# Kernel tuning notes

Hardware: AMD Instinct MI355X
Metric: run time of the kernel (lower is better)

The kernel has to match this reference:

```python
import jax, jax.numpy as jnp
import numpy as np

HEADS = 8
DIM_HEAD = 32
GSS = 3
SCALE = DIM_HEAD ** -0.5
LN_EPS = 1e-5


def setup_inputs() -> dict:
    key = jax.random.key(0)
    ks = jax.random.split(key, 5)
    B, C, H, W = 16, 256, 96, 96
    inner = HEADS * DIM_HEAD  # 256
    return {
        "x": jax.random.normal(ks[0], (B, C, H, W), jnp.float32),
        "w_qkv": jax.random.normal(ks[1], (inner * 3, C), jnp.float32) * 0.02,
        "group_tokens": jax.random.normal(ks[2], (C,), jnp.float32),
        "ln_gamma": jnp.ones((DIM_HEAD,), jnp.float32),
        "ln_beta": jnp.zeros((DIM_HEAD,), jnp.float32),
        "w_qk": jax.random.normal(ks[3], (inner * 2, inner), jnp.float32) * 0.02,
        "b_qk": jnp.zeros((inner * 2,), jnp.float32),
        "w_out": jax.random.normal(ks[4], (C, inner), jnp.float32) * 0.02,
        "b_out": jnp.zeros((C,), jnp.float32),
    }


def reference(x, w_qkv, group_tokens, ln_gamma, ln_beta, w_qk, b_qk, w_out, b_out):
    B, C, H, W = x.shape
    g, h, d = GSS, HEADS, DIM_HEAD
    X, Y = H // g, W // g
    n_groups = X * Y
    bg = B * n_groups
    win = g * g  # 9 tokens per spatial window

    # 'b c (h g1) (w g2) -> (b h w) c (g1 g2)'
    xg = x.reshape(B, C, X, g, Y, g).transpose(0, 2, 4, 1, 3, 5).reshape(bg, C, win)
    # prepend learned group token
    tok = jnp.broadcast_to(group_tokens[None, :, None], (bg, C, 1))
    xg = jnp.concatenate([tok, xg], axis=-1)

    # 1x1 conv QKV projection
    qkv = jnp.einsum('oc,bcn->bon', w_qkv, xg)
    q, k, v = jnp.split(qkv, 3, axis=1)

    def to_heads(t):  # 'b (h d) n -> b h n d'
        return t.reshape(bg, h, d, win + 1).transpose(0, 1, 3, 2)
    q, k, v = map(to_heads, (q, k, v))

    dots = jnp.einsum('bhid,bhjd->bhij', q * SCALE, k)
    attn = jax.nn.softmax(dots, axis=-1)
    out = jnp.einsum('bhij,bhjd->bhid', attn, v)

    gt = out[:, :, 0]    # [bg, h, d] group tokens
    gf = out[:, :, 1:]

    # '(b x y) h d -> b h (x y) d'
    gt = gt.reshape(B, n_groups, h, d).transpose(0, 2, 1, 3)
    # '(b x y) h n d -> b h (x y) n d'
    gf = gf.reshape(B, n_groups, h, win, d).transpose(0, 2, 1, 3, 4)

    # group_tokens_to_qk: LayerNorm(d) -> GELU -> 1x1 conv on (h d) channels
    mu = gt.mean(axis=-1, keepdims=True)
    var = gt.var(axis=-1, keepdims=True)
    gtn = (gt - mu) * jax.lax.rsqrt(var + LN_EPS) * ln_gamma + ln_beta
    gtn = jax.nn.gelu(gtn, approximate=False)
    # 'b h n c -> b (h c) n'
    t = gtn.transpose(0, 1, 3, 2).reshape(B, h * d, n_groups)
    qk = jnp.einsum('oc,bcn->bon', w_qk, t) + b_qk[None, :, None]
    # 'b (h c) n -> b h n c'
    qk = qk.reshape(B, h, 2 * d, n_groups).transpose(0, 1, 3, 2)
    w_q, w_k = jnp.split(qk, 2, axis=-1)

    # stage-2 hierarchical attention over group tokens
    w_dots = jnp.einsum('bhid,bhjd->bhij', w_q * SCALE, w_k)
    w_attn = jax.nn.softmax(w_dots, axis=-1)
    agg = jnp.einsum('bhij,bhjwd->bhiwd', w_attn, gf)

    # 'b h (x y) (g1 g2) d -> b (h d) (x g1) (y g2)'
    fmap = agg.reshape(B, h, X, Y, g, g, d).transpose(0, 1, 6, 2, 4, 3, 5)
    fmap = fmap.reshape(B, h * d, H, W)

    return jnp.einsum('oc,bchw->bohw', w_out, fmap) + b_out[None, :, None, None]
```

## Files before the change

### kernel.cpp

```cpp
#include <hip/hip_runtime.h>
#include <cmath>

namespace {
constexpr int kNH = 8;
constexpr int kNG = 1024;
constexpr float kScale = 0.17677669529663687f;
}

typedef short  bf16x8 __attribute__((ext_vector_type(8)));
typedef short  bf16x4 __attribute__((ext_vector_type(4)));
typedef float  f32x4  __attribute__((ext_vector_type(4)));

__device__ __forceinline__ unsigned short f2b(float f) {
  unsigned int u = __builtin_bit_cast(unsigned int, f);
  u += 0x7fffu + ((u >> 16) & 1u);
  return (unsigned short)(u >> 16);
}
__device__ __forceinline__ float b2f(unsigned short h) {
  unsigned int u = ((unsigned int)h) << 16;
  return __builtin_bit_cast(float, u);
}
__device__ __forceinline__ int swc(int row, int col) {
  return col ^ (((row >> 3) & 3) << 3);
}

__global__ void __launch_bounds__(256) k_wcvt(const float* __restrict__ w_qkv,
                                              const float* __restrict__ w_out,
                                              unsigned short* __restrict__ wb,
                                              unsigned short* __restrict__ w_hi,
                                              unsigned short* __restrict__ w_lo) {
  int i = blockIdx.x * 256 + threadIdx.x;
  if (i < 196608) {
    wb[i] = f2b(w_qkv[i]);
  } else {
    int k = i - 196608;
    float v = w_out[k];
    unsigned short h = f2b(v);
    w_hi[k] = h;
    w_lo[k] = f2b(v - b2f(h));
  }
}

__global__ void __launch_bounds__(256) k_tok(const float* __restrict__ w_qkv,
                                             const float* __restrict__ gtok,
                                             unsigned short* __restrict__ tok_b) {
  int o = blockIdx.x * 256 + threadIdx.x;
  if (o < 768) {
    float s = 0.f;
    for (int c = 0; c < 256; ++c) s += w_qkv[o * 256 + c] * gtok[c];
    tok_b[o] = f2b(s);
  }
}

__global__ void __launch_bounds__(256, 2)
k_xt(const float* __restrict__ x, unsigned short* __restrict__ xt, int b0) {
  __shared__ short Lt[64][72];
  const int tid = threadIdx.x;
  const int bid = blockIdx.x;
  const int bb = bid / 576;
  const int r2 = bid - bb * 576;
  const int ct = r2 / 144;
  const int ptile = r2 - ct * 144;
  const int c0 = ct * 64, p0 = ptile * 64;
  const float* xb = x + ((size_t)((b0 + bb) * 256 + c0)) * 9216 + p0;
#pragma unroll
  for (int i = 0; i < 16; ++i) {
    int idx = i * 256 + tid;
    int c = idx >> 6, p = idx & 63;
    Lt[c][p] = (short)f2b(xb[(size_t)c * 9216 + p]);
  }
  __syncthreads();
  unsigned short* xto = xt + ((size_t)bb * 9216 + p0) * 256 + c0;
#pragma unroll
  for (int i = 0; i < 2; ++i) {
    int t = i * 256 + tid;
    int p = t & 63, oc = t >> 6;
    bf16x8 v8;
#pragma unroll
    for (int e = 0; e < 8; ++e) v8[e] = Lt[oc * 8 + e][p];
    *(bf16x8*)&xto[(size_t)p * 256 + oc * 8] = v8;
  }
}

__global__ void __launch_bounds__(256, 4)
k_qkv(const unsigned short* __restrict__ w_bf, const unsigned short* __restrict__ xt,
      unsigned short* __restrict__ qkv) {
  const int tid = threadIdx.x;
  const int N = gridDim.x;
  const int lg = (blockIdx.x & 7) * (N >> 3) + (blockIdx.x >> 3);
  const int pt = lg / 6;
  const int ot = lg - pt * 6;
  const int o0 = ot * 128;
  const int wv = tid >> 6, lane = tid & 63, ln = lane & 15, qq = lane >> 4;
  const int ow = (wv >> 1) * 64, pw = (wv & 1) * 64;
  const size_t prow = (size_t)pt * 128 + pw;
  const unsigned short* xbase = xt + (prow + ln) * 256;
  const unsigned short* wbase = w_bf + (size_t)(o0 + ow + ln) * 256;

  f32x4 acc[4][4];
#pragma unroll
  for (int mf = 0; mf < 4; ++mf)
#pragma unroll
    for (int nf = 0; nf < 4; ++nf) acc[mf][nf] = {0.f, 0.f, 0.f, 0.f};

  for (int ks = 0; ks < 8; ++ks) {
    const int co = ks * 32 + qq * 8;
    bf16x8 bfr[4], afr[4];
#pragma unroll
    for (int nf = 0; nf < 4; ++nf) bfr[nf] = *(const bf16x8*)&xbase[(size_t)nf * 4096 + co];
#pragma unroll
    for (int mf = 0; mf < 4; ++mf) afr[mf] = *(const bf16x8*)&wbase[(size_t)mf * 4096 + co];
#pragma unroll
    for (int mf = 0; mf < 4; ++mf)
#pragma unroll
      for (int nf = 0; nf < 4; ++nf)
        acc[mf][nf] = __builtin_amdgcn_mfma_f32_16x16x32_bf16(afr[mf], bfr[nf], acc[mf][nf], 0, 0, 0);
  }
#pragma unroll
  for (int mf = 0; mf < 4; ++mf)
#pragma unroll
    for (int nf = 0; nf < 4; ++nf) {
      bf16x4 sv;
#pragma unroll
      for (int r = 0; r < 4; ++r) sv[r] = (short)f2b(acc[mf][nf][r]);
      *(bf16x4*)&qkv[(prow + nf * 16 + ln) * 768 + o0 + ow + mf * 16 + qq * 4] = sv;
    }
}

__global__ void __launch_bounds__(256, 3)
k_attn(const unsigned short* __restrict__ qkv, const unsigned short* __restrict__ tok_b,
       const float* __restrict__ ln_g, const float* __restrict__ ln_b,
       unsigned short* __restrict__ t_b, unsigned short* __restrict__ gf_t, int b0) {
  __shared__ __align__(16) short smem[23040];
  short* vt = smem;
  short* pl = smem + 20480;

  const int tid = threadIdx.x;
  const int N = gridDim.x;
  const int lg = (blockIdx.x & 7) * (N >> 3) + (blockIdx.x >> 3);
  const int bb = lg >> 9;
  const int b  = b0 + bb;
  const int n0 = (lg & 511) * 2;
  const int wv = tid >> 6, lane = tid & 63, ln = lane & 15, qq = lane >> 4;
  const int grp = wv >> 1;
  const int n = n0 + grp;
  const size_t brow = (size_t)bb * 9216;

  {
    bf16x8 z8 = {0, 0, 0, 0, 0, 0, 0, 0};
    for (int i = 0; i < 12; ++i) {
      int off = (i * 256 + tid) * 8;
      if (off < 23040) *(bf16x8*)&smem[off] = z8;
    }
  }
  __syncthreads();

  for (int it = 0; it < 9; ++it) {
    int t = it * 256 + tid;
    if (t < 2304) {
      int win = t >= 1152 ? 1 : 0;
      int rem = t - win * 1152;
      int pix = rem >> 7, dp = rem & 127, d = dp * 2;
      int nn = n0 + win;
      int gx = nn >> 5, gy = nn & 31;
      int gi = (pix * 11) >> 5, gj = pix - 3 * gi;
      int p = (gx * 3 + gi) * 96 + gy * 3 + gj;
      unsigned int u = *(const unsigned int*)&qkv[(brow + p) * 768 + 512 + d];
      int col = pix + 1;
      int r0 = (win << 8) + d;
      vt[r0 * 40 + swc(r0, col)] = (short)(u & 0xffffu);
      vt[(r0 + 1) * 40 + swc(r0 + 1, col)] = (short)(u >> 16);
    }
  }
#pragma unroll
  for (int i = 0; i < 2; ++i) {
    int t = i * 256 + tid;
    vt[t * 40 + swc(t, 0)] = (short)tok_b[512 + (t & 255)];
  }
  __syncthreads();

  const unsigned short* rowq;
  {
    bool isPix = (ln >= 1 && ln <= 9);
    int pix = ln - 1;
    int gi = isPix ? ((pix * 11) >> 5) : 0;
    int gj = isPix ? (pix - 3 * gi) : 0;
    int gx = n >> 5, gy = n & 31;
    int p = (gx * 3 + gi) * 96 + gy * 3 + gj;
    rowq = isPix ? qkv + (brow + p) * 768 + qq * 8 : tok_b + qq * 8;
  }

  f32x4 z = {0.f, 0.f, 0.f, 0.f};
  for (int tt = 0; tt < 4; ++tt) {
    int hh = (wv & 1) * 4 + tt;
    bf16x8 aq = *(const bf16x8*)&rowq[hh * 32];
    bf16x8 bk = *(const bf16x8*)&rowq[256 + hh * 32];
    f32x4 s = __builtin_amdgcn_mfma_f32_16x16x32_bf16(aq, bk, z, 0, 0, 0);

    float pr[4], sm[4];
#pragma unroll
    for (int r = 0; r < 4; ++r) {
      float sv = s[r] * kScale;
      if (ln >= 10) sv = -1e30f;
      float mx = sv;
#pragma unroll
      for (int d = 1; d < 16; d <<= 1) mx = fmaxf(mx, __shfl_xor(mx, d));
      pr[r] = __expf(sv - mx);
      float t2 = pr[r];
#pragma unroll
      for (int d = 1; d < 16; d <<= 1) t2 += __shfl_xor(t2, d);
      sm[r] = t2;
    }
#pragma unroll
    for (int r = 0; r < 4; ++r)
      pl[wv * 640 + (qq * 4 + r) * 40 + ln] = (short)f2b(pr[r]);

    bf16x8 ap = *(const bf16x8*)&pl[wv * 640 + ln * 40 + qq * 8];
    int rv0 = (grp << 8) + hh * 32 + ln;
    int rv1 = rv0 + 16;
    bf16x8 v0 = *(const bf16x8*)&vt[rv0 * 40 + swc(rv0, qq * 8)];
    bf16x8 v1 = *(const bf16x8*)&vt[rv1 * 40 + swc(rv1, qq * 8)];
    f32x4 o0 = __builtin_amdgcn_mfma_f32_16x16x32_bf16(ap, v0, z, 0, 0, 0);
    f32x4 o1 = __builtin_amdgcn_mfma_f32_16x16x32_bf16(ap, v1, z, 0, 0, 0);

    if (qq == 0) {
      float inv0 = 1.f / sm[0];
      float va = o0[0] * inv0, vb = o1[0] * inv0;
      float ssum = va + vb;
#pragma unroll
      for (int d = 1; d < 16; d <<= 1) ssum += __shfl_xor(ssum, d);
      float mu = ssum * (1.f / 32.f);
      float dva = va - mu, dvb = vb - mu;
      float vsum = dva * dva + dvb * dvb;
#pragma unroll
      for (int d = 1; d < 16; d <<= 1) vsum += __shfl_xor(vsum, d);
      float ri = rsqrtf(vsum * (1.f / 32.f) + 1e-5f);
      float g0 = dva * ri * ln_g[ln] + ln_b[ln];
      float g1 = dvb * ri * ln_g[16 + ln] + ln_b[16 + ln];
      float e0 = 0.5f * g0 * (1.f + erff(g0 * 0.70710678118654752f));
      float e1 = 0.5f * g1 * (1.f + erff(g1 * 0.70710678118654752f));
      size_t tb = ((size_t)(b * 1024 + n)) * 256 + hh * 32 + ln;
      t_b[tb] = f2b(e0);
      t_b[tb + 16] = f2b(e1);
    }
#pragma unroll
    for (int r = 0; r < 4; ++r) {
      int i = qq * 4 + r;
      if (i >= 1 && i <= 9) {
        float inv = 1.f / sm[r];
        size_t base = ((size_t)((b * 8 + hh) * 288) + (i - 1) * 32 + ln) * 1024 + n;
        gf_t[base] = f2b(o0[r] * inv);
        gf_t[base + 16 * 1024] = f2b(o1[r] * inv);
      }
    }
  }
}

__global__ void __launch_bounds__(256, 2)
k_qk(const unsigned short* __restrict__ t_b, const float* __restrict__ w_qk,
     const float* __restrict__ b_qk, unsigned short* __restrict__ wq_b,
     unsigned short* __restrict__ wk_b) {
  __shared__ float t_l[128][33];
  __shared__ float w_l[64][33];
  int tid = threadIdx.x;
  int bid = blockIdx.x;
  int b = bid >> 6;
  int h = (bid >> 3) & 7;
  int nt = bid & 7;
  int n_base = nt * 128;
  int te = tid & 15, tn = tid >> 4;
  float accq[4][8] = {};
  for (int c0 = 0; c0 < 256; c0 += 32) {
    for (int i = 0; i < 16; ++i) {
      int nl = i * 8 + (tid >> 5);
      t_l[nl][tid & 31] = b2f(t_b[((size_t)(b * kNG) + n_base + nl) * 256 + c0 + (tid & 31)]);
    }
    for (int i = 0; i < 8; ++i) {
      int e = i * 8 + (tid >> 5);
      w_l[e][tid & 31] = w_qk[(size_t)(h * 64 + e) * 256 + c0 + (tid & 31)];
    }
    __syncthreads();
    for (int cc = 0; cc < 32; ++cc) {
      float wvv[4], tvv[8];
#pragma unroll
      for (int i = 0; i < 4; ++i) wvv[i] = w_l[te + 16 * i][cc];
#pragma unroll
      for (int j = 0; j < 8; ++j) tvv[j] = t_l[tn + 16 * j][cc];
#pragma unroll
      for (int i = 0; i < 4; ++i)
#pragma unroll
        for (int j = 0; j < 8; ++j) accq[i][j] += wvv[i] * tvv[j];
    }
    __syncthreads();
  }
#pragma unroll
  for (int i = 0; i < 4; ++i) {
    int e = te + 16 * i;
    float bias = b_qk[h * 64 + e];
#pragma unroll
    for (int j = 0; j < 8; ++j) {
      int n = n_base + tn + 16 * j;
      float v = accq[i][j] + bias;
      size_t idx = (((size_t)b * kNH + h) * kNG + n) * 32;
      if (e < 32) wq_b[idx + e] = f2b(v * kScale);
      else        wk_b[idx + (e - 32)] = f2b(v);
    }
  }
}

__global__ void __launch_bounds__(256, 3)
k_flash(const unsigned short* __restrict__ wq_b, const unsigned short* __restrict__ wk_b,
        const unsigned short* __restrict__ gf_t, unsigned short* __restrict__ agg_b) {
  __shared__ __align__(16) short vt[12800];
  __shared__ __align__(16) short pl[2560];
  __shared__ float al_l[64];
  __shared__ float lrow_l[64];

  const int tid = threadIdx.x;
  const int bid0 = blockIdx.x;
  const int xcd = bid0 & 7;
  const int s   = bid0 >> 3;
  const int bh  = xcd + 8 * (s >> 4);
  const int qt  = s & 15;
  const int wv = tid >> 6;
  const int lane = tid & 63;
  const int ln = lane & 15;
  const int qq = lane >> 4;
  const int d0 = wv * 80;

  bf16x8 aq = *(const bf16x8*)&wq_b[(size_t)(bh * 1024 + qt * 64 + wv * 16 + ln) * 32 + qq * 8];

  f32x4 accv[4][5];
  float mrow[4], lrow[4];
#pragma unroll
  for (int mf = 0; mf < 4; ++mf)
#pragma unroll
    for (int nf = 0; nf < 5; ++nf) accv[mf][nf] = {0.f, 0.f, 0.f, 0.f};
#pragma unroll
  for (int r = 0; r < 4; ++r) { mrow[r] = -1e30f; lrow[r] = 0.f; }

  for (int i = tid; i < 1280; i += 256) vt[11520 + i] = 0;

  for (int kt = 0; kt < 32; ++kt) {
    __syncthreads();
#pragma unroll
    for (int ii = 0; ii < 5; ++ii) {
      int i = ii * 256 + tid;
      if (i < 1152) {
        int d = i >> 2, c = (i & 3) * 8;
        bf16x8 g = *(const bf16x8*)&gf_t[((size_t)(bh * 288 + d)) * 1024 + kt * 32 + c];
        *(bf16x8*)&vt[d * 40 + c] = g;
      }
    }
    f32x4 z = {0.f, 0.f, 0.f, 0.f};
    bf16x8 kf0 = *(const bf16x8*)&wk_b[(size_t)(bh * 1024 + kt * 32 + ln) * 32 + qq * 8];
    bf16x8 kf1 = *(const bf16x8*)&wk_b[(size_t)(bh * 1024 + kt * 32 + 16 + ln) * 32 + qq * 8];
    f32x4 s0v = __builtin_amdgcn_mfma_f32_16x16x32_bf16(aq, kf0, z, 0, 0, 0);
    f32x4 s1v = __builtin_amdgcn_mfma_f32_16x16x32_bf16(aq, kf1, z, 0, 0, 0);
#pragma unroll
    for (int r = 0; r < 4; ++r) {
      float a0 = s0v[r], a1 = s1v[r];
      float tm = fmaxf(a0, a1);
#pragma unroll
      for (int d = 1; d < 16; d <<= 1) tm = fmaxf(tm, __shfl_xor(tm, d));
      float nm = fmaxf(mrow[r], tm);
      float al = __expf(mrow[r] - nm);
      mrow[r] = nm;
      float p0 = __expf(a0 - nm), p1 = __expf(a1 - nm);
      float ts = p0 + p1;
#pragma unroll
      for (int d = 1; d < 16; d <<= 1) ts += __shfl_xor(ts, d);
      lrow[r] = lrow[r] * al + ts;
      int row = wv * 16 + qq * 4 + r;
      pl[row * 40 + ln] = (short)f2b(p0);
      pl[row * 40 + 16 + ln] = (short)f2b(p1);
      if (ln == 0) al_l[row] = al;
    }
    __syncthreads();
#pragma unroll
    for (int mf = 0; mf < 4; ++mf)
#pragma unroll
      for (int r = 0; r < 4; ++r) {
        float alv = al_l[mf * 16 + qq * 4 + r];
#pragma unroll
        for (int nf = 0; nf < 5; ++nf) accv[mf][nf][r] *= alv;
      }
    bf16x8 ap[4];
#pragma unroll
    for (int mf = 0; mf < 4; ++mf)
      ap[mf] = *(const bf16x8*)&pl[(mf * 16 + ln) * 40 + qq * 8];
    __builtin_amdgcn_s_setprio(1);
#pragma unroll
    for (int nf = 0; nf < 5; ++nf) {
      bf16x8 vf = *(const bf16x8*)&vt[(d0 + nf * 16 + ln) * 40 + qq * 8];
#pragma unroll
      for (int mf = 0; mf < 4; ++mf)
        accv[mf][nf] = __builtin_amdgcn_mfma_f32_16x16x32_bf16(ap[mf], vf, accv[mf][nf], 0, 0, 0);
    }
    __builtin_amdgcn_s_setprio(0);
  }
#pragma unroll
  for (int r = 0; r < 4; ++r)
    if (ln == 0) lrow_l[wv * 16 + qq * 4 + r] = lrow[r];
  __syncthreads();
#pragma unroll
  for (int mf = 0; mf < 4; ++mf)
#pragma unroll
    for (int r = 0; r < 4; ++r) {
      float linv = 1.f / lrow_l[mf * 16 + qq * 4 + r];
      int row = qt * 64 + mf * 16 + qq * 4 + r;
#pragma unroll
      for (int nf = 0; nf < 5; ++nf) {
        int d = d0 + nf * 16 + ln;
        if (d < 288)
          agg_b[((size_t)(bh * 1024) + row) * 288 + d] = f2b(accv[mf][nf][r] * linv);
      }
    }
}

__global__ void __launch_bounds__(256, 2)
k_out(const unsigned short* __restrict__ agg_b,
      const unsigned short* __restrict__ w_hi, const unsigned short* __restrict__ w_lo,
      const float* __restrict__ b_out, float* __restrict__ out) {
  const int tid = threadIdx.x;
  const int bid = blockIdx.x;
  const int b = bid / 144;
  const int pt = bid - b * 144;
  const int p_base = pt * 64;
  const int wv = tid >> 6, lane = tid & 63, ln = lane & 15, qq = lane >> 4;
  const int obase = wv * 64;

  size_t vbase[4];
#pragma unroll
  for (int nf = 0; nf < 4; ++nf) {
    int p = p_base + nf * 16 + ln;
    int hh2 = p / 96, ww2 = p - hh2 * 96;
    int xg = hh2 / 3, gi = hh2 - xg * 3;
    int yg = ww2 / 3, gj = ww2 - yg * 3;
    int nn = xg * 32 + yg, w = gi * 3 + gj;
    vbase[nf] = ((size_t)b * 8 * 1024 + nn) * 288 + w * 32 + qq * 8;
  }

  f32x4 acc[4][4];
#pragma unroll
  for (int mf = 0; mf < 4; ++mf)
#pragma unroll
    for (int nf = 0; nf < 4; ++nf) acc[mf][nf] = {0.f, 0.f, 0.f, 0.f};

  for (int ks = 0; ks < 8; ++ks) {
    bf16x8 bfr[4];
#pragma unroll
    for (int nf = 0; nf < 4; ++nf)
      bfr[nf] = *(const bf16x8*)&agg_b[vbase[nf] + (size_t)ks * 294912];
#pragma unroll
    for (int mf = 0; mf < 4; ++mf) {
      int o = obase + mf * 16 + ln;
      bf16x8 ah = *(const bf16x8*)&w_hi[o * 256 + ks * 32 + qq * 8];
      bf16x8 al = *(const bf16x8*)&w_lo[o * 256 + ks * 32 + qq * 8];
#pragma unroll
      for (int nf = 0; nf < 4; ++nf) {
        acc[mf][nf] = __builtin_amdgcn_mfma_f32_16x16x32_bf16(ah, bfr[nf], acc[mf][nf], 0, 0, 0);
        acc[mf][nf] = __builtin_amdgcn_mfma_f32_16x16x32_bf16(al, bfr[nf], acc[mf][nf], 0, 0, 0);
      }
    }
  }
#pragma unroll
  for (int mf = 0; mf < 4; ++mf) {
#pragma unroll
    for (int r = 0; r < 4; ++r) {
      int o = obase + mf * 16 + qq * 4 + r;
      float bias = b_out[o];
#pragma unroll
      for (int nf = 0; nf < 4; ++nf) {
        int p = p_base + nf * 16 + ln;
        out[((size_t)b * 256 + o) * 9216 + p] = acc[mf][nf][r] + bias;
      }
    }
  }
}

extern "C" void kernel_launch(void* const* d_in, const int* in_sizes, int n_in,
                              void* d_out, int out_size, void* d_ws, size_t ws_size,
                              hipStream_t stream) {
  const float* x     = (const float*)d_in[0];
  const float* w_qkv = (const float*)d_in[1];
  const float* gtok  = (const float*)d_in[2];
  const float* ln_g  = (const float*)d_in[3];
  const float* ln_b  = (const float*)d_in[4];
  const float* w_qk  = (const float*)d_in[5];
  const float* b_qk  = (const float*)d_in[6];
  const float* w_out = (const float*)d_in[7];
  const float* b_out = (const float*)d_in[8];
  float* out = (float*)d_out;

  unsigned short* ws   = (unsigned short*)d_ws;
  unsigned short* w_bf = ws;
  unsigned short* w_hi = ws + 196608;
  unsigned short* w_lo = ws + 262144;
  unsigned short* tok  = ws + 327680;
  unsigned short* t_b  = ws + 328704;
  unsigned short* wq_b = ws + 4523008;
  unsigned short* wk_b = ws + 8717312;
  unsigned short* gf_t = ws + 12911616;
  unsigned short* R    = ws + 50660352;

  auto need = [](int NBv) -> size_t {
    size_t reg = (size_t)NBv * 9437184ull;
    if (reg < 37748736ull) reg = 37748736ull;
    return (50660352ull + reg) * 2ull;
  };
  int NB = 4;
  if (ws_size >= need(16)) NB = 16;
  else if (ws_size >= need(8)) NB = 8;

  unsigned short* qkv = R;
  unsigned short* xt  = R + (size_t)NB * 7077888ull;
  unsigned short* agg_b = R;

  k_wcvt<<<1024, 256, 0, stream>>>(w_qkv, w_out, w_bf, w_hi, w_lo);
  k_tok<<<3, 256, 0, stream>>>(w_qkv, gtok, tok);
  for (int c = 0; c < 16 / NB; ++c) {
    int b0 = c * NB;
    k_xt<<<NB * 576, 256, 0, stream>>>(x, xt, b0);
    k_qkv<<<NB * 432, 256, 0, stream>>>(w_bf, xt, qkv);
    k_attn<<<NB * 512, 256, 0, stream>>>(qkv, tok, ln_g, ln_b, t_b, gf_t, b0);
  }
  k_qk<<<1024, 256, 0, stream>>>(t_b, w_qk, b_qk, wq_b, wk_b);
  k_flash<<<2048, 256, 0, stream>>>(wq_b, wk_b, gf_t, agg_b);
  k_out<<<2304, 256, 0, stream>>>(agg_b, w_hi, w_lo, b_out, out);
}
```

Before: 1.256 ms.

## Use split-bf16 MFMA for qk projection; restructure flash to per-wave V from global with lazy rescale

The qk projection moves from scalar FP32 LDS-tiled FMAs to MFMA bf16, with w_qk split into hi/lo bf16 halves to keep accuracy. The flash kernel drops the shared V staging and block-wide barriers. Each wave now owns 16 query rows across all 288 output columns, reads V fragments straight from global memory, and keeps its P tile in per-wave LDS. Rescaling of the accumulator is skipped whenever the running max grows by at most 8, which cuts exp and multiply work. The trade-off is heavier global traffic for V (each wave re-reads it), more accumulator registers, and small bf16 overflow/precision risk from the deferred max.

After: 2.528 ms. 2.01x slower.

```diff
diff --git a/kernel.cpp b/kernel.cpp
--- a/kernel.cpp
+++ b/kernel.cpp
@@ -39,6 +39,16 @@
     w_hi[k] = h;
     w_lo[k] = f2b(v - b2f(h));
   }
+}
+
+__global__ void __launch_bounds__(256) k_wqkcvt(const float* __restrict__ w_qk,
+                                                unsigned short* __restrict__ hi,
+                                                unsigned short* __restrict__ lo) {
+  int i = blockIdx.x * 256 + threadIdx.x;
+  float v = w_qk[i];
+  unsigned short h = f2b(v);
+  hi[i] = h;
+  lo[i] = f2b(v - b2f(h));
 }
 
 __global__ void __launch_bounds__(256) k_tok(const float* __restrict__ w_qkv,
@@ -256,65 +266,65 @@
   }
 }
 
-__global__ void __launch_bounds__(256, 2)
-k_qk(const unsigned short* __restrict__ t_b, const float* __restrict__ w_qk,
-     const float* __restrict__ b_qk, unsigned short* __restrict__ wq_b,
-     unsigned short* __restrict__ wk_b) {
-  __shared__ float t_l[128][33];
-  __shared__ float w_l[64][33];
-  int tid = threadIdx.x;
-  int bid = blockIdx.x;
-  int b = bid >> 6;
-  int h = (bid >> 3) & 7;
-  int nt = bid & 7;
-  int n_base = nt * 128;
-  int te = tid & 15, tn = tid >> 4;
-  float accq[4][8] = {};
-  for (int c0 = 0; c0 < 256; c0 += 32) {
-    for (int i = 0; i < 16; ++i) {
-      int nl = i * 8 + (tid >> 5);
-      t_l[nl][tid & 31] = b2f(t_b[((size_t)(b * kNG) + n_base + nl) * 256 + c0 + (tid & 31)]);
-    }
-    for (int i = 0; i < 8; ++i) {
-      int e = i * 8 + (tid >> 5);
-      w_l[e][tid & 31] = w_qk[(size_t)(h * 64 + e) * 256 + c0 + (tid & 31)];
-    }
-    __syncthreads();
-    for (int cc = 0; cc < 32; ++cc) {
-      float wvv[4], tvv[8];
-#pragma unroll
-      for (int i = 0; i < 4; ++i) wvv[i] = w_l[te + 16 * i][cc];
-#pragma unroll
-      for (int j = 0; j < 8; ++j) tvv[j] = t_l[tn + 16 * j][cc];
-#pragma unroll
-      for (int i = 0; i < 4; ++i)
-#pragma unroll
-        for (int j = 0; j < 8; ++j) accq[i][j] += wvv[i] * tvv[j];
-    }
-    __syncthreads();
-  }
-#pragma unroll
-  for (int i = 0; i < 4; ++i) {
-    int e = te + 16 * i;
-    float bias = b_qk[h * 64 + e];
-#pragma unroll
-    for (int j = 0; j < 8; ++j) {
-      int n = n_base + tn + 16 * j;
-      float v = accq[i][j] + bias;
-      size_t idx = (((size_t)b * kNH + h) * kNG + n) * 32;
-      if (e < 32) wq_b[idx + e] = f2b(v * kScale);
-      else        wk_b[idx + (e - 32)] = f2b(v);
-    }
-  }
-}
-
-__global__ void __launch_bounds__(256, 3)
+__global__ void __launch_bounds__(256, 4)
+k_qk(const unsigned short* __restrict__ t_b, const unsigned short* __restrict__ wqk_hi,
+     const unsigned short* __restrict__ wqk_lo, const float* __restrict__ b_qk,
+     unsigned short* __restrict__ wq_b, unsigned short* __restrict__ wk_b) {
+  const int tid = threadIdx.x;
+  const int bid = blockIdx.x;
+  const int lg = (bid & 7) * 64 + (bid >> 3);
+  const int h = lg & 7;
+  const int bnt = lg >> 3;
+  const int b = bnt >> 2, nt = bnt & 3;
+  const int wv = tid >> 6, lane = tid & 63, ln = lane & 15, qq = lane >> 4;
+  const int n0 = nt * 256 + wv * 64;
+  const unsigned short* tb  = t_b + ((size_t)b * 1024 + n0 + ln) * 256;
+  const unsigned short* whb = wqk_hi + (size_t)(h * 64 + ln) * 256;
+  const unsigned short* wlb = wqk_lo + (size_t)(h * 64 + ln) * 256;
+
+  f32x4 acc[4][4];
+#pragma unroll
+  for (int mf = 0; mf < 4; ++mf)
+#pragma unroll
+    for (int nf = 0; nf < 4; ++nf) acc[mf][nf] = {0.f, 0.f, 0.f, 0.f};
+
+  for (int ks = 0; ks < 8; ++ks) {
+    const int co = ks * 32 + qq * 8;
+    bf16x8 bfr[4];
+#pragma unroll
+    for (int nf = 0; nf < 4; ++nf) bfr[nf] = *(const bf16x8*)&tb[(size_t)nf * 4096 + co];
+#pragma unroll
+    for (int mf = 0; mf < 4; ++mf) {
+      bf16x8 ah = *(const bf16x8*)&whb[(size_t)mf * 4096 + co];
+      bf16x8 al = *(const bf16x8*)&wlb[(size_t)mf * 4096 + co];
+#pragma unroll
+      for (int nf = 0; nf < 4; ++nf) {
+        acc[mf][nf] = __builtin_amdgcn_mfma_f32_16x16x32_bf16(ah, bfr[nf], acc[mf][nf], 0, 0, 0);
+        acc[mf][nf] = __builtin_amdgcn_mfma_f32_16x16x32_bf16(al, bfr[nf], acc[mf][nf], 0, 0, 0);
+      }
+    }
+  }
+#pragma unroll
+  for (int mf = 0; mf < 4; ++mf)
+#pragma unroll
+    for (int r = 0; r < 4; ++r) {
+      int e = mf * 16 + qq * 4 + r;
+      float bias = b_qk[h * 64 + e];
+#pragma unroll
+      for (int nf = 0; nf < 4; ++nf) {
+        int n = n0 + nf * 16 + ln;
+        float v = acc[mf][nf][r] + bias;
+        size_t idx = (((size_t)b * kNH + h) * kNG + n) * 32;
+        if (e < 32) wq_b[idx + e] = f2b(v * kScale);
+        else        wk_b[idx + (e - 32)] = f2b(v);
+      }
+    }
+}
+
+__global__ void __launch_bounds__(256, 4)
 k_flash(const unsigned short* __restrict__ wq_b, const unsigned short* __restrict__ wk_b,
         const unsigned short* __restrict__ gf_t, unsigned short* __restrict__ agg_b) {
-  __shared__ __align__(16) short vt[12800];
-  __shared__ __align__(16) short pl[2560];
-  __shared__ float al_l[64];
-  __shared__ float lrow_l[64];
+  __shared__ __align__(16) short pl[4 * 640];
 
   const int tid = threadIdx.x;
   const int bid0 = blockIdx.x;
@@ -322,100 +332,88 @@
   const int s   = bid0 >> 3;
   const int bh  = xcd + 8 * (s >> 4);
   const int qt  = s & 15;
-  const int wv = tid >> 6;
-  const int lane = tid & 63;
-  const int ln = lane & 15;
-  const int qq = lane >> 4;
-  const int d0 = wv * 80;
+  const int wv = tid >> 6, lane = tid & 63, ln = lane & 15, qq = lane >> 4;
+  short* plw = pl + wv * 640;
 
   bf16x8 aq = *(const bf16x8*)&wq_b[(size_t)(bh * 1024 + qt * 64 + wv * 16 + ln) * 32 + qq * 8];
-
-  f32x4 accv[4][5];
+  const unsigned short* kb = wk_b + (size_t)bh * 32768;
+  const unsigned short* vb = gf_t + (size_t)bh * 294912 + (size_t)ln * 1024;
+
+  f32x4 accv[18];
+#pragma unroll
+  for (int nf = 0; nf < 18; ++nf) accv[nf] = {0.f, 0.f, 0.f, 0.f};
   float mrow[4], lrow[4];
 #pragma unroll
-  for (int mf = 0; mf < 4; ++mf)
-#pragma unroll
-    for (int nf = 0; nf < 5; ++nf) accv[mf][nf] = {0.f, 0.f, 0.f, 0.f};
-#pragma unroll
   for (int r = 0; r < 4; ++r) { mrow[r] = -1e30f; lrow[r] = 0.f; }
 
-  for (int i = tid; i < 1280; i += 256) vt[11520 + i] = 0;
-
   for (int kt = 0; kt < 32; ++kt) {
-    __syncthreads();
-#pragma unroll
-    for (int ii = 0; ii < 5; ++ii) {
-      int i = ii * 256 + tid;
-      if (i < 1152) {
-        int d = i >> 2, c = (i & 3) * 8;
-        bf16x8 g = *(const bf16x8*)&gf_t[((size_t)(bh * 288 + d)) * 1024 + kt * 32 + c];
-        *(bf16x8*)&vt[d * 40 + c] = g;
-      }
-    }
+    const unsigned short* kp = kb + (kt * 32 + ln) * 32 + qq * 8;
+    bf16x8 kf0 = *(const bf16x8*)kp;
+    bf16x8 kf1 = *(const bf16x8*)(kp + 512);
     f32x4 z = {0.f, 0.f, 0.f, 0.f};
-    bf16x8 kf0 = *(const bf16x8*)&wk_b[(size_t)(bh * 1024 + kt * 32 + ln) * 32 + qq * 8];
-    bf16x8 kf1 = *(const bf16x8*)&wk_b[(size_t)(bh * 1024 + kt * 32 + 16 + ln) * 32 + qq * 8];
     f32x4 s0v = __builtin_amdgcn_mfma_f32_16x16x32_bf16(aq, kf0, z, 0, 0, 0);
     f32x4 s1v = __builtin_amdgcn_mfma_f32_16x16x32_bf16(aq, kf1, z, 0, 0, 0);
+
+    float tmx[4];
+    bool small = true;
 #pragma unroll
     for (int r = 0; r < 4; ++r) {
-      float a0 = s0v[r], a1 = s1v[r];
-      float tm = fmaxf(a0, a1);
+      float tm = fmaxf(s0v[r], s1v[r]);
 #pragma unroll
       for (int d = 1; d < 16; d <<= 1) tm = fmaxf(tm, __shfl_xor(tm, d));
-      float nm = fmaxf(mrow[r], tm);
-      float al = __expf(mrow[r] - nm);
-      mrow[r] = nm;
-      float p0 = __expf(a0 - nm), p1 = __expf(a1 - nm);
-      float ts = p0 + p1;
-#pragma unroll
-      for (int d = 1; d < 16; d <<= 1) ts += __shfl_xor(ts, d);
-      lrow[r] = lrow[r] * al + ts;
-      int row = wv * 16 + qq * 4 + r;
-      pl[row * 40 + ln] = (short)f2b(p0);
-      pl[row * 40 + 16 + ln] = (short)f2b(p1);
-      if (ln == 0) al_l[row] = al;
-    }
-    __syncthreads();
-#pragma unroll
-    for (int mf = 0; mf < 4; ++mf)
+      tmx[r] = tm;
+      small = small && (tm - mrow[r] <= 8.f);
+    }
+    if (__all(small)) {
 #pragma unroll
       for (int r = 0; r < 4; ++r) {
-        float alv = al_l[mf * 16 + qq * 4 + r];
-#pragma unroll
-        for (int nf = 0; nf < 5; ++nf) accv[mf][nf][r] *= alv;
-      }
-    bf16x8 ap[4];
-#pragma unroll
-    for (int mf = 0; mf < 4; ++mf)
-      ap[mf] = *(const bf16x8*)&pl[(mf * 16 + ln) * 40 + qq * 8];
+        float p0 = __expf(s0v[r] - mrow[r]), p1 = __expf(s1v[r] - mrow[r]);
+        float ts = p0 + p1;
+#pragma unroll
+        for (int d = 1; d < 16; d <<= 1) ts += __shfl_xor(ts, d);
+        lrow[r] += ts;
+        plw[(qq * 4 + r) * 40 + ln] = (short)f2b(p0);
+        plw[(qq * 4 + r) * 40 + 16 + ln] = (short)f2b(p1);
+      }
+    } else {
+      float alr[4];
+#pragma unroll
+      for (int r = 0; r < 4; ++r) {
+        float nm = fmaxf(mrow[r], tmx[r]);
+        alr[r] = __expf(mrow[r] - nm);
+        mrow[r] = nm;
+        float p0 = __expf(s0v[r] - nm), p1 = __expf(s1v[r] - nm);
+        float ts = p0 + p1;
+#pragma unroll
+        for (int d = 1; d < 16; d <<= 1) ts += __shfl_xor(ts, d);
+        lrow[r] = lrow[r] * alr[r] + ts;
+        plw[(qq * 4 + r) * 40 + ln] = (short)f2b(p0);
+        plw[(qq * 4 + r) * 40 + 16 + ln] = (short)f2b(p1);
+      }
+#pragma unroll
+      for (int nf = 0; nf < 18; ++nf)
+#pragma unroll
+        for (int r = 0; r < 4; ++r) accv[nf][r] *= alr[r];
+    }
+
+    bf16x8 ap = *(const bf16x8*)&plw[ln * 40 + qq * 8];
+    const unsigned short* vp = vb + kt * 32 + qq * 8;
     __builtin_amdgcn_s_setprio(1);
 #pragma unroll
-    for (int nf = 0; nf < 5; ++nf) {
-      bf16x8 vf = *(const bf16x8*)&vt[(d0 + nf * 16 + ln) * 40 + qq * 8];
-#pragma unroll
-      for (int mf = 0; mf < 4; ++mf)
-        accv[mf][nf] = __builtin_amdgcn_mfma_f32_16x16x32_bf16(ap[mf], vf, accv[mf][nf], 0, 0, 0);
+    for (int nf = 0; nf < 18; ++nf) {
+      bf16x8 vf = *(const bf16x8*)&vp[(size_t)nf * 16384];
+      accv[nf] = __builtin_amdgcn_mfma_f32_16x16x32_bf16(ap, vf, accv[nf], 0, 0, 0);
     }
     __builtin_amdgcn_s_setprio(0);
   }
 #pragma unroll
-  for (int r = 0; r < 4; ++r)
-    if (ln == 0) lrow_l[wv * 16 + qq * 4 + r] = lrow[r];
-  __syncthreads();
-#pragma unroll
-  for (int mf = 0; mf < 4; ++mf)
-#pragma unroll
-    for (int r = 0; r < 4; ++r) {
-      float linv = 1.f / lrow_l[mf * 16 + qq * 4 + r];
-      int row = qt * 64 + mf * 16 + qq * 4 + r;
-#pragma unroll
-      for (int nf = 0; nf < 5; ++nf) {
-        int d = d0 + nf * 16 + ln;
-        if (d < 288)
-          agg_b[((size_t)(bh * 1024) + row) * 288 + d] = f2b(accv[mf][nf][r] * linv);
-      }
-    }
+  for (int r = 0; r < 4; ++r) {
+    float linv = 1.f / lrow[r];
+    int row = qt * 64 + wv * 16 + qq * 4 + r;
+#pragma unroll
+    for (int nf = 0; nf < 18; ++nf)
+      agg_b[((size_t)bh * 1024 + row) * 288 + nf * 16 + ln] = f2b(accv[nf][r] * linv);
+  }
 }
 
 __global__ void __launch_bounds__(256, 2)
@@ -516,6 +514,8 @@
   unsigned short* qkv = R;
   unsigned short* xt  = R + (size_t)NB * 7077888ull;
   unsigned short* agg_b = R;
+  unsigned short* wqk_hi = xt;
+  unsigned short* wqk_lo = xt + 131072;
 
   k_wcvt<<<1024, 256, 0, stream>>>(w_qkv, w_out, w_bf, w_hi, w_lo);
   k_tok<<<3, 256, 0, stream>>>(w_qkv, gtok, tok);
@@ -525,7 +525,8 @@
     k_qkv<<<NB * 432, 256, 0, stream>>>(w_bf, xt, qkv);
     k_attn<<<NB * 512, 256, 0, stream>>>(qkv, tok, ln_g, ln_b, t_b, gf_t, b0);
   }
-  k_qk<<<1024, 256, 0, stream>>>(t_b, w_qk, b_qk, wq_b, wk_b);
+  k_wqkcvt<<<512, 256, 0, stream>>>(w_qk, wqk_hi, wqk_lo);
+  k_qk<<<512, 256, 0, stream>>>(t_b, wqk_hi, wqk_lo, b_qk, wq_b, wk_b);
   k_flash<<<2048, 256, 0, stream>>>(wq_b, wk_b, gf_t, agg_b);
   k_out<<<2304, 256, 0, stream>>>(agg_b, w_hi, w_lo, b_out, out);
 }
```
